# Performance work log

Measured on AMD Instinct MI355X. Metric: run time of the kernel, lower is better.

The kernel has to match this reference:

```python
import jax, jax.numpy as jnp
import numpy as np

N = 20000          # num_node
E = 160000         # num edges (avg degree 8)
IN_N = 64          # in_features_node
IN_E = 32          # in_features_edge
HN = 64            # nhid_node
HE = 64            # nhid_edge
KAPPA = 0.9
ITERS = 8          # fixed Picard iterations for the equilibrium solve


def setup_inputs() -> dict:
    key = jax.random.key(0)
    ks = jax.random.split(key, 16)
    f32 = jnp.float32

    def w(k, shape, fan_in):
        return (jax.random.normal(k, shape, dtype=f32) / np.sqrt(fan_in)).astype(f32)

    return {
        # graph structure (int constants)
        "R": jax.random.randint(ks[0], (E,), 0, N),   # receiver node per edge
        "S": jax.random.randint(ks[1], (E,), 0, N),   # sender node per edge
        "H": jax.random.randint(ks[2], (E,), 0, N),   # edge->node aggregation index
        # features (features-first layout, as in the torch code)
        "node_data": jax.random.normal(ks[3], (IN_N, N), dtype=f32),
        "Ra_data": jax.random.normal(ks[4], (IN_E, E), dtype=f32),
        # INECN_Layer parameters
        "W_es": w(ks[5], (HE, HN), HN),      # sender-message weight
        "W_er": w(ks[6], (HE, HN), HN),      # receiver-message weight
        "Omega_e": w(ks[7], (HE, IN_E), IN_E),
        "Wn": w(ks[8], (HN, HN), HN),        # implicit node-state weight
        "Bm": w(ks[9], (HN, HE), HE),        # edge->node mixing
        "Omega_n": w(ks[10], (HN, IN_N), IN_N),
        # dense head (V_0: nhid->nhid, V_1: nhid->in_features_node)
        "V0_w": w(ks[11], (HN, HN), HN),
        "V0_b": jnp.zeros((HN,), dtype=f32),
        "V1_w": w(ks[12], (IN_N, HN), HN),
        "V1_b": jnp.zeros((IN_N,), dtype=f32),
    }


def reference(R, S, H, node_data, Ra_data, W_es, W_er, Omega_e, Wn, Bm,
              Omega_n, V0_w, V0_b, V1_w, V1_b):
    # spectral-norm style contraction: ||kappa * Wn / ||Wn|||| <= kappa (adj_rho = 1)
    Wn_hat = (KAPPA * Wn) / jnp.maximum(jnp.linalg.norm(Wn), 1.0)

    bias_e = Omega_e @ Ra_data        # [HE, E] injected edge features
    bias_n = Omega_n @ node_data      # [HN, N] injected node features

    def step(X, _):
        # edge update: messages from sender/receiver node states
        He_logits = W_es @ X[:, S] + W_er @ X[:, R] + bias_e      # [HE, E]
        He = jax.nn.relu(He_logits)
        # aggregate edge states back to nodes
        agg = jax.ops.segment_sum(He.T, H, num_segments=N).T      # [HE, N] -> [HE, N]
        # implicit node update (contraction => convergent fixed point)
        X_new = jax.nn.relu(Wn_hat @ X + Bm @ agg + bias_n)       # [HN, N]
        return X_new, None

    X0 = jnp.zeros((HN, N), dtype=node_data.dtype)
    X, _ = jax.lax.scan(step, X0, None, length=ITERS)

    # final edge states / logits at the (approximate) fixed point
    He_logits3 = W_es @ X[:, S] + W_er @ X[:, R] + bias_e         # [HE, E]
    He = jax.nn.relu(He_logits3)

    # dense head: x = V_1(dropout(relu(V_0(x.T))))  (eval mode: dropout = identity)
    x = X.T                                                        # [N, HN]
    x = jax.nn.relu(x @ V0_w.T + V0_b)                             # [N, HN]
    x = x @ V1_w.T + V1_b                                          # [N, IN_N]
    return (x, He, He_logits3)
```

## Files before the change

kernel.cpp:

```cpp
#include <hip/hip_runtime.h>
#include <math.h>

#define KAPPA 0.9f
#define ST 68
#define TN 32

typedef unsigned short u16;

__device__ __forceinline__ float relu_f(float v) { return fmaxf(v, 0.0f); }
__device__ __forceinline__ float bf_lo(unsigned u) { return __uint_as_float(u << 16); }
__device__ __forceinline__ float bf_hi(unsigned u) { return __uint_as_float(u & 0xFFFF0000u); }
__device__ __forceinline__ u16 f2bf(float x) {
  unsigned u = __float_as_uint(x);
  return (u16)((u + 0x7FFFu + ((u >> 16) & 1u)) >> 16);
}
__device__ __forceinline__ unsigned pack2(float a, float b) {
  return (unsigned)f2bf(a) | ((unsigned)f2bf(b) << 16);
}

__global__ __launch_bounds__(256) void wnhat_kernel(const float* __restrict__ Wn,
                                                    float* __restrict__ Wn_hat) {
  __shared__ float red[4];
  int t = threadIdx.x;
  float v[16];
  float s = 0.f;
#pragma unroll
  for (int j = 0; j < 16; ++j) { v[j] = Wn[t + 256 * j]; s += v[j] * v[j]; }
#pragma unroll
  for (int off = 32; off > 0; off >>= 1) s += __shfl_down(s, off, 64);
  if ((t & 63) == 0) red[t >> 6] = s;
  __syncthreads();
  float norm = sqrtf(red[0] + red[1] + red[2] + red[3]);
  float scale = KAPPA / fmaxf(norm, 1.0f);
#pragma unroll
  for (int j = 0; j < 16; ++j) Wn_hat[t + 256 * j] = v[j] * scale;
}

__global__ __launch_bounds__(256) void bias_n_kernel(const float* __restrict__ node_data,
                                                     const float* __restrict__ Om_n,
                                                     float* __restrict__ bias_n, int N) {
  __shared__ float NdT[64][ST];
  __shared__ float Om[64][ST];
  int t = threadIdx.x;
  int n_base = blockIdx.x * 64;
#pragma unroll
  for (int j = 0; j < 16; ++j) {
    int f = t + 256 * j;
    int r = f >> 6, c = f & 63;
    float val = (n_base + c < N) ? node_data[(size_t)r * N + n_base + c] : 0.f;
    NdT[c][r] = val;
    Om[r][c] = Om_n[f];
  }
  __syncthreads();
  int ni = t & 15, h4 = (t >> 4) * 4;
  float acc[4][4] = {};
#pragma unroll 4
  for (int k = 0; k < 64; k += 4) {
    float4 a[4], w[4];
#pragma unroll
    for (int i = 0; i < 4; ++i) a[i] = *(const float4*)&NdT[ni + 16 * i][k];
#pragma unroll
    for (int j = 0; j < 4; ++j) w[j] = *(const float4*)&Om[h4 + j][k];
#pragma unroll
    for (int i = 0; i < 4; ++i)
#pragma unroll
      for (int j = 0; j < 4; ++j)
        acc[i][j] += a[i].x * w[j].x + a[i].y * w[j].y + a[i].z * w[j].z + a[i].w * w[j].w;
  }
#pragma unroll
  for (int i = 0; i < 4; ++i) {
    int n = n_base + ni + 16 * i;
    if (n < N) {
      float4 o = make_float4(acc[i][0], acc[i][1], acc[i][2], acc[i][3]);
      *(float4*)&bias_n[(size_t)n * 64 + h4] = o;
    }
  }
}

__global__ void hist_kernel(const int* __restrict__ H, int* __restrict__ count, int E) {
  int e = blockIdx.x * 256 + threadIdx.x;
  if (e < E) atomicAdd(&count[H[e]], 1);
}

__global__ __launch_bounds__(256) void scan_kernel(int* count, int* row_off, int* cursor,
                                                   int N, int E) {
  __shared__ int offs[256];
  __shared__ int sums[256];
  int t = threadIdx.x;
  int chunk = (N + 255) / 256;
  int lo = t * chunk, hi = min(lo + chunk, N);
  int s = 0;
  for (int n = lo; n < hi; ++n) s += count[n];
  sums[t] = s;
  __syncthreads();
  if (t == 0) {
    int run = 0;
    for (int i = 0; i < 256; ++i) { offs[i] = run; run += sums[i]; }
  }
  __syncthreads();
  int run = offs[t];
  for (int n = lo; n < hi; ++n) {
    int c = count[n];
    row_off[n] = run;
    cursor[n] = run;
    run += c;
  }
  if (t == 0) row_off[N] = E;
}

__global__ void scatter_kernel(const int* __restrict__ H, const int* __restrict__ S,
                               const int* __restrict__ R, int* cursor,
                               int* __restrict__ Ss, int* __restrict__ Rs,
                               int* __restrict__ inv_perm, int E) {
  int e = blockIdx.x * 256 + threadIdx.x;
  if (e < E) {
    int h = H[e];
    int pos = atomicAdd(&cursor[h], 1);
    Ss[pos] = S[e];
    Rs[pos] = R[e];
    inv_perm[e] = pos;
  }
}

__global__ __launch_bounds__(256) void bias_build_kernel(const float* __restrict__ Ra,
                                                         const float* __restrict__ Om_e,
                                                         const int* __restrict__ inv_perm,
                                                         u16* __restrict__ bias_sb, int E) {
  __shared__ float OmT[64][36];
  __shared__ float RaT[64][36];
  int t = threadIdx.x;
  int e_base = blockIdx.x * 64;
#pragma unroll
  for (int j = 0; j < 8; ++j) {
    int f = t + 256 * j;
    int r = f >> 5, c = f & 31;
    OmT[r][c] = Om_e[f];
  }
#pragma unroll
  for (int j = 0; j < 8; ++j) {
    int f = t + 256 * j;
    int r = f >> 6, c = f & 63;
    int ee = e_base + c;
    RaT[c][r] = (ee < E) ? Ra[(size_t)r * E + ee] : 0.f;
  }
  __syncthreads();
  int ei = t & 15, h4 = (t >> 4) * 4;
  float acc[4][4] = {};
#pragma unroll 4
  for (int jj = 0; jj < 32; jj += 4) {
    float4 ra[4], om[4];
#pragma unroll
    for (int i = 0; i < 4; ++i) ra[i] = *(const float4*)&RaT[ei + 16 * i][jj];
#pragma unroll
    for (int j = 0; j < 4; ++j) om[j] = *(const float4*)&OmT[h4 + j][jj];
#pragma unroll
    for (int i = 0; i < 4; ++i)
#pragma unroll
      for (int j = 0; j < 4; ++j)
        acc[i][j] += ra[i].x * om[j].x + ra[i].y * om[j].y + ra[i].z * om[j].z +
                     ra[i].w * om[j].w;
  }
#pragma unroll
  for (int i = 0; i < 4; ++i) {
    int e = e_base + ei + 16 * i;
    if (e < E) {
      int p = inv_perm[e];
      uint2 o;
      o.x = pack2(acc[i][0], acc[i][1]);
      o.y = pack2(acc[i][2], acc[i][3]);
      *(uint2*)&bias_sb[((size_t)p << 6) + h4] = o;
    }
  }
}

template <int FIRST, int LAST>
__global__ __launch_bounds__(256) void iter_kernel(
    const float* __restrict__ X, const u16* __restrict__ MSb_in,
    const u16* __restrict__ MRb_in, const u16* __restrict__ bias_sb,
    const int* __restrict__ Ss, const int* __restrict__ Rs,
    const int* __restrict__ row_off, const float* __restrict__ bias_n,
    const float* __restrict__ Wn_hat, const float* __restrict__ Bm,
    const float* __restrict__ W_es, const float* __restrict__ W_er,
    const float* __restrict__ V0_w, const float* __restrict__ V0_b,
    const float* __restrict__ V1_w, const float* __restrict__ V1_b,
    float* __restrict__ Xout, u16* __restrict__ MSb_out,
    u16* __restrict__ MRb_out, float* __restrict__ head_out, int N) {
  __shared__ float Wa[64][ST], Wb[64][ST];
  __shared__ float Xsh[TN][ST], Ash[TN][ST];
  __shared__ float b0s[64], b1s[64];
  int t = threadIdx.x;
  int n_base = blockIdx.x * TN;
#pragma unroll
  for (int j = 0; j < 16; ++j) {
    int f = t + 256 * j;
    int r = f >> 6, c = f & 63;
    Wa[r][c] = Wn_hat[f];
    Wb[r][c] = Bm[f];
  }
  int n8 = t >> 3;
  int q8 = t & 7;
  int nd = n_base + n8;
  bool ok = nd < N;
  if (!FIRST) {
    float4 x0 = make_float4(0, 0, 0, 0), x1 = x0;
    if (ok) {
      x0 = *(const float4*)&X[(size_t)nd * 64 + q8 * 8];
      x1 = *(const float4*)&X[(size_t)nd * 64 + q8 * 8 + 4];
    }
    *(float4*)&Xsh[n8][q8 * 8] = x0;
    *(float4*)&Xsh[n8][q8 * 8 + 4] = x1;
  }
  float a[8] = {};
  if (ok) {
    int r0 = row_off[nd], r1 = row_off[nd + 1];
    for (int p = r0; p < r1; ++p) {
      uint4 bv = *(const uint4*)&bias_sb[((size_t)p << 6) + q8 * 8];
      if (FIRST) {
        a[0] += relu_f(bf_lo(bv.x)); a[1] += relu_f(bf_hi(bv.x));
        a[2] += relu_f(bf_lo(bv.y)); a[3] += relu_f(bf_hi(bv.y));
        a[4] += relu_f(bf_lo(bv.z)); a[5] += relu_f(bf_hi(bv.z));
        a[6] += relu_f(bf_lo(bv.w)); a[7] += relu_f(bf_hi(bv.w));
      } else {
        int s = Ss[p], r = Rs[p];
        uint4 mv = *(const uint4*)&MSb_in[((size_t)s << 6) + q8 * 8];
        uint4 rv = *(const uint4*)&MRb_in[((size_t)r << 6) + q8 * 8];
        a[0] += relu_f(bf_lo(mv.x) + bf_lo(rv.x) + bf_lo(bv.x));
        a[1] += relu_f(bf_hi(mv.x) + bf_hi(rv.x) + bf_hi(bv.x));
        a[2] += relu_f(bf_lo(mv.y) + bf_lo(rv.y) + bf_lo(bv.y));
        a[3] += relu_f(bf_hi(mv.y) + bf_hi(rv.y) + bf_hi(bv.y));
        a[4] += relu_f(bf_lo(mv.z) + bf_lo(rv.z) + bf_lo(bv.z));
        a[5] += relu_f(bf_hi(mv.z) + bf_hi(rv.z) + bf_hi(bv.z));
        a[6] += relu_f(bf_lo(mv.w) + bf_lo(rv.w) + bf_lo(bv.w));
        a[7] += relu_f(bf_hi(mv.w) + bf_hi(rv.w) + bf_hi(bv.w));
      }
    }
  }
  *(float4*)&Ash[n8][q8 * 8] = make_float4(a[0], a[1], a[2], a[3]);
  *(float4*)&Ash[n8][q8 * 8 + 4] = make_float4(a[4], a[5], a[6], a[7]);
  __syncthreads();
  int ni = t & 15, h4 = (t >> 4) * 4;
  float acc[2][4] = {};
#pragma unroll 4
  for (int k = 0; k < 64; k += 4) {
    float4 xv[2], av[2], wv[4], bv[4];
#pragma unroll
    for (int i = 0; i < 2; ++i) {
      if (!FIRST) xv[i] = *(const float4*)&Xsh[ni + 16 * i][k];
      av[i] = *(const float4*)&Ash[ni + 16 * i][k];
    }
#pragma unroll
    for (int j = 0; j < 4; ++j) {
      wv[j] = *(const float4*)&Wa[h4 + j][k];
      bv[j] = *(const float4*)&Wb[h4 + j][k];
    }
#pragma unroll
    for (int i = 0; i < 2; ++i)
#pragma unroll
      for (int j = 0; j < 4; ++j) {
        float v = av[i].x * bv[j].x + av[i].y * bv[j].y + av[i].z * bv[j].z +
                  av[i].w * bv[j].w;
        if (!FIRST)
          v += xv[i].x * wv[j].x + xv[i].y * wv[j].y + xv[i].z * wv[j].z +
               xv[i].w * wv[j].w;
        acc[i][j] += v;
      }
  }
  __syncthreads();
#pragma unroll
  for (int i = 0; i < 2; ++i) {
    int nn = n_base + ni + 16 * i;
    float4 bb = make_float4(0, 0, 0, 0);
    if (nn < N) bb = *(const float4*)&bias_n[(size_t)nn * 64 + h4];
    float x0 = relu_f(acc[i][0] + bb.x);
    float x1 = relu_f(acc[i][1] + bb.y);
    float x2 = relu_f(acc[i][2] + bb.z);
    float x3 = relu_f(acc[i][3] + bb.w);
    if (!LAST && nn < N)
      *(float4*)&Xout[(size_t)nn * 64 + h4] = make_float4(x0, x1, x2, x3);
    *(float4*)&Xsh[ni + 16 * i][h4] = make_float4(x0, x1, x2, x3);
  }
#pragma unroll
  for (int j = 0; j < 16; ++j) {
    int f = t + 256 * j;
    int r = f >> 6, c = f & 63;
    Wa[r][c] = W_es[f];
    Wb[r][c] = W_er[f];
  }
  __syncthreads();
  {
    float ma[2][4] = {}, ra[2][4] = {};
#pragma unroll 4
    for (int k = 0; k < 64; k += 4) {
      float4 xv[2], ws[4], wr[4];
#pragma unroll
      for (int i = 0; i < 2; ++i) xv[i] = *(const float4*)&Xsh[ni + 16 * i][k];
#pragma unroll
      for (int j = 0; j < 4; ++j) {
        ws[j] = *(const float4*)&Wa[h4 + j][k];
        wr[j] = *(const float4*)&Wb[h4 + j][k];
      }
#pragma unroll
      for (int i = 0; i < 2; ++i)
#pragma unroll
        for (int j = 0; j < 4; ++j) {
          ma[i][j] += xv[i].x * ws[j].x + xv[i].y * ws[j].y + xv[i].z * ws[j].z +
                      xv[i].w * ws[j].w;
          ra[i][j] += xv[i].x * wr[j].x + xv[i].y * wr[j].y + xv[i].z * wr[j].z +
                      xv[i].w * wr[j].w;
        }
    }
#pragma unroll
    for (int i = 0; i < 2; ++i) {
      int nn = n_base + ni + 16 * i;
      if (nn < N) {
        uint2 om, orr;
        om.x = pack2(ma[i][0], ma[i][1]);
        om.y = pack2(ma[i][2], ma[i][3]);
        orr.x = pack2(ra[i][0], ra[i][1]);
        orr.y = pack2(ra[i][2], ra[i][3]);
        *(uint2*)&MSb_out[((size_t)nn << 6) + h4] = om;
        *(uint2*)&MRb_out[((size_t)nn << 6) + h4] = orr;
      }
    }
  }
  if (LAST) {
    __syncthreads();
#pragma unroll
    for (int j = 0; j < 16; ++j) {
      int f = t + 256 * j;
      int r = f >> 6, c = f & 63;
      Wa[r][c] = V0_w[f];
      Wb[r][c] = V1_w[f];
    }
    if (t < 64) b0s[t] = V0_b[t];
    else if (t < 128) b1s[t - 64] = V1_b[t - 64];
    __syncthreads();
    float c1[2][4] = {};
#pragma unroll 4
    for (int k = 0; k < 64; k += 4) {
      float4 xv[2], wv[4];
#pragma unroll
      for (int i = 0; i < 2; ++i) xv[i] = *(const float4*)&Xsh[ni + 16 * i][k];
#pragma unroll
      for (int j = 0; j < 4; ++j) wv[j] = *(const float4*)&Wa[h4 + j][k];
#pragma unroll
      for (int i = 0; i < 2; ++i)
#pragma unroll
        for (int j = 0; j < 4; ++j)
          c1[i][j] += xv[i].x * wv[j].x + xv[i].y * wv[j].y + xv[i].z * wv[j].z +
                      xv[i].w * wv[j].w;
    }
    __syncthreads();
#pragma unroll
    for (int i = 0; i < 2; ++i) {
      float4 o;
      o.x = relu_f(c1[i][0] + b0s[h4 + 0]);
      o.y = relu_f(c1[i][1] + b0s[h4 + 1]);
      o.z = relu_f(c1[i][2] + b0s[h4 + 2]);
      o.w = relu_f(c1[i][3] + b0s[h4 + 3]);
      *(float4*)&Xsh[ni + 16 * i][h4] = o;
    }
    __syncthreads();
    float c2[2][4] = {};
#pragma unroll 4
    for (int k = 0; k < 64; k += 4) {
      float4 xv[2], wv[4];
#pragma unroll
      for (int i = 0; i < 2; ++i) xv[i] = *(const float4*)&Xsh[ni + 16 * i][k];
#pragma unroll
      for (int j = 0; j < 4; ++j) wv[j] = *(const float4*)&Wb[h4 + j][k];
#pragma unroll
      for (int i = 0; i < 2; ++i)
#pragma unroll
        for (int j = 0; j < 4; ++j)
          c2[i][j] += xv[i].x * wv[j].x + xv[i].y * wv[j].y + xv[i].z * wv[j].z +
                      xv[i].w * wv[j].w;
    }
#pragma unroll
    for (int i = 0; i < 2; ++i) {
      int nn = n_base + ni + 16 * i;
      if (nn < N) {
        float4 o;
        o.x = c2[i][0] + b1s[h4 + 0];
        o.y = c2[i][1] + b1s[h4 + 1];
        o.z = c2[i][2] + b1s[h4 + 2];
        o.w = c2[i][3] + b1s[h4 + 3];
        *(float4*)&head_out[(size_t)nn * 64 + h4] = o;
      }
    }
  }
}

__global__ __launch_bounds__(256) void edge_final_kernel(
    const u16* __restrict__ MSb, const u16* __restrict__ MRb,
    const int* __restrict__ S, const int* __restrict__ R,
    const float* __restrict__ Om_e, const float* __restrict__ Ra,
    float* __restrict__ He_out, float* __restrict__ Hel_out, int E) {
  __shared__ float T[64][ST];
  __shared__ float pool2[4608];
  int t = threadIdx.x;
  int e_base = blockIdx.x * 64;
#pragma unroll
  for (int j = 0; j < 8; ++j) {
    int f = t + 256 * j;
    int r = f >> 5, c = f & 31;
    pool2[r * 36 + c] = Om_e[f];
  }
#pragma unroll
  for (int j = 0; j < 8; ++j) {
    int f = t + 256 * j;
    int r = f >> 6, c = f & 63;
    int e2 = e_base + c;
    pool2[2304 + c * 36 + r] = (e2 < E) ? Ra[(size_t)r * E + e2] : 0.f;
  }
  {
    int e = t >> 2, q = t & 3;
    int ee = e_base + e;
    int ec = (ee < E) ? ee : 0;
    int s = S[ec], r = R[ec];
    const u16* mp = &MSb[((size_t)s << 6) + q * 16];
    const u16* rp = &MRb[((size_t)r << 6) + q * 16];
    uint4 m0 = *(const uint4*)mp;
    uint4 m1 = *(const uint4*)(mp + 8);
    uint4 r0 = *(const uint4*)rp;
    uint4 r1 = *(const uint4*)(rp + 8);
    float* tp = &T[e][q * 16];
    tp[0] = bf_lo(m0.x) + bf_lo(r0.x);
    tp[1] = bf_hi(m0.x) + bf_hi(r0.x);
    tp[2] = bf_lo(m0.y) + bf_lo(r0.y);
    tp[3] = bf_hi(m0.y) + bf_hi(r0.y);
    tp[4] = bf_lo(m0.z) + bf_lo(r0.z);
    tp[5] = bf_hi(m0.z) + bf_hi(r0.z);
    tp[6] = bf_lo(m0.w) + bf_lo(r0.w);
    tp[7] = bf_hi(m0.w) + bf_hi(r0.w);
    tp[8] = bf_lo(m1.x) + bf_lo(r1.x);
    tp[9] = bf_hi(m1.x) + bf_hi(r1.x);
    tp[10] = bf_lo(m1.y) + bf_lo(r1.y);
    tp[11] = bf_hi(m1.y) + bf_hi(r1.y);
    tp[12] = bf_lo(m1.z) + bf_lo(r1.z);
    tp[13] = bf_hi(m1.z) + bf_hi(r1.z);
    tp[14] = bf_lo(m1.w) + bf_lo(r1.w);
    tp[15] = bf_hi(m1.w) + bf_hi(r1.w);
  }
  __syncthreads();
  int ei = t & 15, h4 = (t >> 4) * 4;
  float acc[4][4] = {};
#pragma unroll 4
  for (int jj = 0; jj < 32; jj += 4) {
    float4 ra[4], om[4];
#pragma unroll
    for (int i = 0; i < 4; ++i)
      ra[i] = *(const float4*)&pool2[2304 + (ei + 16 * i) * 36 + jj];
#pragma unroll
    for (int j = 0; j < 4; ++j) om[j] = *(const float4*)&pool2[(h4 + j) * 36 + jj];
#pragma unroll
    for (int i = 0; i < 4; ++i)
#pragma unroll
      for (int j = 0; j < 4; ++j)
        acc[i][j] += ra[i].x * om[j].x + ra[i].y * om[j].y + ra[i].z * om[j].z +
                     ra[i].w * om[j].w;
  }
#pragma unroll
  for (int i = 0; i < 4; ++i) {
    float4 tv = *(const float4*)&T[ei + 16 * i][h4];
    acc[i][0] += tv.x;
    acc[i][1] += tv.y;
    acc[i][2] += tv.z;
    acc[i][3] += tv.w;
  }
  __syncthreads();
#pragma unroll
  for (int i = 0; i < 4; ++i)
#pragma unroll
    for (int j = 0; j < 4; ++j)
      pool2[(ei + 16 * i) * 65 + h4 + j] = acc[i][j];
  __syncthreads();
  {
    int e4 = (t & 15) * 4, h0 = t >> 4;
#pragma unroll
    for (int rep = 0; rep < 4; ++rep) {
      int h = h0 + 16 * rep;
      float4 v;
      v.x = pool2[(e4 + 0) * 65 + h];
      v.y = pool2[(e4 + 1) * 65 + h];
      v.z = pool2[(e4 + 2) * 65 + h];
      v.w = pool2[(e4 + 3) * 65 + h];
      size_t idx = (size_t)h * E + e_base + e4;
      if (e_base + e4 < E) {
        *(float4*)&Hel_out[idx] = v;
        float4 u = make_float4(relu_f(v.x), relu_f(v.y), relu_f(v.z), relu_f(v.w));
        *(float4*)&He_out[idx] = u;
      }
    }
  }
}

extern "C" void kernel_launch(void* const* d_in, const int* in_sizes, int n_in,
                              void* d_out, int out_size, void* d_ws, size_t ws_size,
                              hipStream_t stream) {
  const int* R = (const int*)d_in[0];
  const int* S = (const int*)d_in[1];
  const int* H = (const int*)d_in[2];
  const float* node_data = (const float*)d_in[3];
  const float* Ra = (const float*)d_in[4];
  const float* W_es = (const float*)d_in[5];
  const float* W_er = (const float*)d_in[6];
  const float* Om_e = (const float*)d_in[7];
  const float* Wn = (const float*)d_in[8];
  const float* Bm = (const float*)d_in[9];
  const float* Om_n = (const float*)d_in[10];
  const float* V0_w = (const float*)d_in[11];
  const float* V0_b = (const float*)d_in[12];
  const float* V1_w = (const float*)d_in[13];
  const float* V1_b = (const float*)d_in[14];
  const int E = in_sizes[0];
  const int N = in_sizes[3] / 64;
  const size_t N64 = (size_t)N * 64;

  float* ws = (float*)d_ws;
  float* Wn_hat = ws;
  float* bias_n = Wn_hat + 4096;
  float* X0 = bias_n + N64;
  float* X1p = X0 + N64;
  u16* MSb_B = (u16*)(X1p + N64);
  u16* MRb_B = MSb_B + N64;
  int* row_off = (int*)(MRb_B + N64);
  int* cursor = row_off + (N + 1);
  int* Ss = cursor + N;
  int* Rs = Ss + E;
  int* inv_perm = Rs + E;

  float* out = (float*)d_out;
  float* out_x = out;
  float* out_He = out + N64;
  float* out_Hel = out_He + (size_t)64 * E;
  u16* bias_sb = (u16*)out_He;
  u16* MSb_A = (u16*)out_Hel;
  u16* MRb_A = MSb_A + N64;

  int nb_node = (N + 63) / 64;
  int nb_iter = (N + TN - 1) / TN;
  int nb_edge = (E + 63) / 64;
  int nb_flat = (E + 255) / 256;

  hipMemsetAsync(cursor, 0, (size_t)N * sizeof(int), stream);
  wnhat_kernel<<<1, 256, 0, stream>>>(Wn, Wn_hat);
  bias_n_kernel<<<nb_node, 256, 0, stream>>>(node_data, Om_n, bias_n, N);
  hist_kernel<<<nb_flat, 256, 0, stream>>>(H, cursor, E);
  scan_kernel<<<1, 256, 0, stream>>>(cursor, row_off, cursor, N, E);
  scatter_kernel<<<nb_flat, 256, 0, stream>>>(H, S, R, cursor, Ss, Rs, inv_perm, E);
  bias_build_kernel<<<nb_edge, 256, 0, stream>>>(Ra, Om_e, inv_perm, bias_sb, E);

  float* Xa = X0;
  float* Xb = X1p;
  const u16* msi = nullptr;
  const u16* mri = nullptr;
  for (int it = 0; it < 8; ++it) {
    u16* mso = (it & 1) ? MSb_B : MSb_A;
    u16* mro = (it & 1) ? MRb_B : MRb_A;
    if (it == 0)
      iter_kernel<1, 0><<<nb_iter, 256, 0, stream>>>(
          Xa, nullptr, nullptr, bias_sb, Ss, Rs, row_off, bias_n, Wn_hat, Bm, W_es, W_er,
          V0_w, V0_b, V1_w, V1_b, Xb, mso, mro, out_x, N);
    else if (it < 7)
      iter_kernel<0, 0><<<nb_iter, 256, 0, stream>>>(
          Xa, msi, mri, bias_sb, Ss, Rs, row_off, bias_n, Wn_hat, Bm, W_es, W_er,
          V0_w, V0_b, V1_w, V1_b, Xb, mso, mro, out_x, N);
    else
      iter_kernel<0, 1><<<nb_iter, 256, 0, stream>>>(
          Xa, msi, mri, bias_sb, Ss, Rs, row_off, bias_n, Wn_hat, Bm, W_es, W_er,
          V0_w, V0_b, V1_w, V1_b, Xb, mso, mro, out_x, N);
    msi = mso;
    mri = mro;
    float* tmp = Xa; Xa = Xb; Xb = tmp;
  }
  edge_final_kernel<<<nb_edge, 256, 0, stream>>>(MSb_B, MRb_B, S, R, Om_e, Ra,
                                                 out_He, out_Hel, E);
}
```

Measured before the change: 486.3 us.

## Split edge aggregation into separate kernel with 4-way per-node edge parallelism

Moves the per-node gather/relu/sum over incoming edges out of the fused iteration kernel into a dedicated aggregation kernel. That kernel gives each node 32 threads, splits its edge list four ways and reduces the partial sums in shared memory, so more gather loads are in flight. It writes an fp32 agg buffer that the node kernel then reads. Sender and receiver indices are also packed into one int2 array. The cost is an extra launch and an extra global round-trip of the agg buffer per iteration.

```diff
diff --git a/kernel.cpp b/kernel.cpp
--- a/kernel.cpp
+++ b/kernel.cpp
@@ -110,14 +110,12 @@
 
 __global__ void scatter_kernel(const int* __restrict__ H, const int* __restrict__ S,
                                const int* __restrict__ R, int* cursor,
-                               int* __restrict__ Ss, int* __restrict__ Rs,
-                               int* __restrict__ inv_perm, int E) {
+                               int2* __restrict__ SRs, int* __restrict__ inv_perm, int E) {
   int e = blockIdx.x * 256 + threadIdx.x;
   if (e < E) {
     int h = H[e];
     int pos = atomicAdd(&cursor[h], 1);
-    Ss[pos] = S[e];
-    Rs[pos] = R[e];
+    SRs[pos] = make_int2(S[e], R[e]);
     inv_perm[e] = pos;
   }
 }
@@ -173,18 +171,67 @@
   }
 }
 
+template <int FIRST>
+__global__ __launch_bounds__(256) void agg_kernel(
+    const u16* __restrict__ MSb_in, const u16* __restrict__ MRb_in,
+    const u16* __restrict__ bias_sb, const int2* __restrict__ SRs,
+    const int* __restrict__ row_off, float* __restrict__ agg, int N) {
+  __shared__ float part[4][8][ST];
+  int t = threadIdx.x;
+  int nl = t >> 5, sp = (t >> 3) & 3, q8 = t & 7;
+  int nd = blockIdx.x * 8 + nl;
+  float a[8] = {};
+  if (nd < N) {
+    int r0 = row_off[nd], r1 = row_off[nd + 1];
+    for (int p = r0 + sp; p < r1; p += 4) {
+      uint4 bv = *(const uint4*)&bias_sb[((size_t)p << 6) + q8 * 8];
+      if (FIRST) {
+        a[0] += relu_f(bf_lo(bv.x)); a[1] += relu_f(bf_hi(bv.x));
+        a[2] += relu_f(bf_lo(bv.y)); a[3] += relu_f(bf_hi(bv.y));
+        a[4] += relu_f(bf_lo(bv.z)); a[5] += relu_f(bf_hi(bv.z));
+        a[6] += relu_f(bf_lo(bv.w)); a[7] += relu_f(bf_hi(bv.w));
+      } else {
+        int2 sr = SRs[p];
+        uint4 mv = *(const uint4*)&MSb_in[((size_t)sr.x << 6) + q8 * 8];
+        uint4 rv = *(const uint4*)&MRb_in[((size_t)sr.y << 6) + q8 * 8];
+        a[0] += relu_f(bf_lo(mv.x) + bf_lo(rv.x) + bf_lo(bv.x));
+        a[1] += relu_f(bf_hi(mv.x) + bf_hi(rv.x) + bf_hi(bv.x));
+        a[2] += relu_f(bf_lo(mv.y) + bf_lo(rv.y) + bf_lo(bv.y));
+        a[3] += relu_f(bf_hi(mv.y) + bf_hi(rv.y) + bf_hi(bv.y));
+        a[4] += relu_f(bf_lo(mv.z) + bf_lo(rv.z) + bf_lo(bv.z));
+        a[5] += relu_f(bf_hi(mv.z) + bf_hi(rv.z) + bf_hi(bv.z));
+        a[6] += relu_f(bf_lo(mv.w) + bf_lo(rv.w) + bf_lo(bv.w));
+        a[7] += relu_f(bf_hi(mv.w) + bf_hi(rv.w) + bf_hi(bv.w));
+      }
+    }
+  }
+  *(float4*)&part[sp][nl][q8 * 8] = make_float4(a[0], a[1], a[2], a[3]);
+  *(float4*)&part[sp][nl][q8 * 8 + 4] = make_float4(a[4], a[5], a[6], a[7]);
+  __syncthreads();
+  if (sp == 0 && nd < N) {
+#pragma unroll
+    for (int u = 0; u < 2; ++u) {
+      float4 s0 = *(const float4*)&part[0][nl][q8 * 8 + 4 * u];
+      float4 s1 = *(const float4*)&part[1][nl][q8 * 8 + 4 * u];
+      float4 s2 = *(const float4*)&part[2][nl][q8 * 8 + 4 * u];
+      float4 s3 = *(const float4*)&part[3][nl][q8 * 8 + 4 * u];
+      float4 o = make_float4(s0.x + s1.x + s2.x + s3.x, s0.y + s1.y + s2.y + s3.y,
+                             s0.z + s1.z + s2.z + s3.z, s0.w + s1.w + s2.w + s3.w);
+      *(float4*)&agg[(size_t)nd * 64 + q8 * 8 + 4 * u] = o;
+    }
+  }
+}
+
 template <int FIRST, int LAST>
-__global__ __launch_bounds__(256) void iter_kernel(
-    const float* __restrict__ X, const u16* __restrict__ MSb_in,
-    const u16* __restrict__ MRb_in, const u16* __restrict__ bias_sb,
-    const int* __restrict__ Ss, const int* __restrict__ Rs,
-    const int* __restrict__ row_off, const float* __restrict__ bias_n,
-    const float* __restrict__ Wn_hat, const float* __restrict__ Bm,
-    const float* __restrict__ W_es, const float* __restrict__ W_er,
-    const float* __restrict__ V0_w, const float* __restrict__ V0_b,
-    const float* __restrict__ V1_w, const float* __restrict__ V1_b,
-    float* __restrict__ Xout, u16* __restrict__ MSb_out,
-    u16* __restrict__ MRb_out, float* __restrict__ head_out, int N) {
+__global__ __launch_bounds__(256) void node_kernel(
+    const float* __restrict__ X, const float* __restrict__ agg,
+    const float* __restrict__ bias_n, const float* __restrict__ Wn_hat,
+    const float* __restrict__ Bm, const float* __restrict__ W_es,
+    const float* __restrict__ W_er, const float* __restrict__ V0_w,
+    const float* __restrict__ V0_b, const float* __restrict__ V1_w,
+    const float* __restrict__ V1_b, float* __restrict__ Xout,
+    u16* __restrict__ MSb_out, u16* __restrict__ MRb_out,
+    float* __restrict__ head_out, int N) {
   __shared__ float Wa[64][ST], Wb[64][ST];
   __shared__ float Xsh[TN][ST], Ash[TN][ST];
   __shared__ float b0s[64], b1s[64];
@@ -210,33 +257,15 @@
     *(float4*)&Xsh[n8][q8 * 8] = x0;
     *(float4*)&Xsh[n8][q8 * 8 + 4] = x1;
   }
-  float a[8] = {};
-  if (ok) {
-    int r0 = row_off[nd], r1 = row_off[nd + 1];
-    for (int p = r0; p < r1; ++p) {
-      uint4 bv = *(const uint4*)&bias_sb[((size_t)p << 6) + q8 * 8];
-      if (FIRST) {
-        a[0] += relu_f(bf_lo(bv.x)); a[1] += relu_f(bf_hi(bv.x));
-        a[2] += relu_f(bf_lo(bv.y)); a[3] += relu_f(bf_hi(bv.y));
-        a[4] += relu_f(bf_lo(bv.z)); a[5] += relu_f(bf_hi(bv.z));
-        a[6] += relu_f(bf_lo(bv.w)); a[7] += relu_f(bf_hi(bv.w));
-      } else {
-        int s = Ss[p], r = Rs[p];
-        uint4 mv = *(const uint4*)&MSb_in[((size_t)s << 6) + q8 * 8];
-        uint4 rv = *(const uint4*)&MRb_in[((size_t)r << 6) + q8 * 8];
-        a[0] += relu_f(bf_lo(mv.x) + bf_lo(rv.x) + bf_lo(bv.x));
-        a[1] += relu_f(bf_hi(mv.x) + bf_hi(rv.x) + bf_hi(bv.x));
-        a[2] += relu_f(bf_lo(mv.y) + bf_lo(rv.y) + bf_lo(bv.y));
-        a[3] += relu_f(bf_hi(mv.y) + bf_hi(rv.y) + bf_hi(bv.y));
-        a[4] += relu_f(bf_lo(mv.z) + bf_lo(rv.z) + bf_lo(bv.z));
-        a[5] += relu_f(bf_hi(mv.z) + bf_hi(rv.z) + bf_hi(bv.z));
-        a[6] += relu_f(bf_lo(mv.w) + bf_lo(rv.w) + bf_lo(bv.w));
-        a[7] += relu_f(bf_hi(mv.w) + bf_hi(rv.w) + bf_hi(bv.w));
-      }
-    }
-  }
-  *(float4*)&Ash[n8][q8 * 8] = make_float4(a[0], a[1], a[2], a[3]);
-  *(float4*)&Ash[n8][q8 * 8 + 4] = make_float4(a[4], a[5], a[6], a[7]);
+  {
+    float4 a0 = make_float4(0, 0, 0, 0), a1 = a0;
+    if (ok) {
+      a0 = *(const float4*)&agg[(size_t)nd * 64 + q8 * 8];
+      a1 = *(const float4*)&agg[(size_t)nd * 64 + q8 * 8 + 4];
+    }
+    *(float4*)&Ash[n8][q8 * 8] = a0;
+    *(float4*)&Ash[n8][q8 * 8 + 4] = a1;
+  }
   __syncthreads();
   int ni = t & 15, h4 = (t >> 4) * 4;
   float acc[2][4] = {};
@@ -526,9 +555,8 @@
   u16* MRb_B = MSb_B + N64;
   int* row_off = (int*)(MRb_B + N64);
   int* cursor = row_off + (N + 1);
-  int* Ss = cursor + N;
-  int* Rs = Ss + E;
-  int* inv_perm = Rs + E;
+  int2* SRs = (int2*)(cursor + N);
+  int* inv_perm = (int*)(SRs + E);
 
   float* out = (float*)d_out;
   float* out_x = out;
@@ -537,9 +565,11 @@
   u16* bias_sb = (u16*)out_He;
   u16* MSb_A = (u16*)out_Hel;
   u16* MRb_A = MSb_A + N64;
+  float* aggf = (float*)(MRb_A + N64);
 
   int nb_node = (N + 63) / 64;
   int nb_iter = (N + TN - 1) / TN;
+  int nb_agg = (N + 7) / 8;
   int nb_edge = (E + 63) / 64;
   int nb_flat = (E + 255) / 256;
 
@@ -548,7 +578,7 @@
   bias_n_kernel<<<nb_node, 256, 0, stream>>>(node_data, Om_n, bias_n, N);
   hist_kernel<<<nb_flat, 256, 0, stream>>>(H, cursor, E);
   scan_kernel<<<1, 256, 0, stream>>>(cursor, row_off, cursor, N, E);
-  scatter_kernel<<<nb_flat, 256, 0, stream>>>(H, S, R, cursor, Ss, Rs, inv_perm, E);
+  scatter_kernel<<<nb_flat, 256, 0, stream>>>(H, S, R, cursor, SRs, inv_perm, E);
   bias_build_kernel<<<nb_edge, 256, 0, stream>>>(Ra, Om_e, inv_perm, bias_sb, E);
 
   float* Xa = X0;
@@ -558,18 +588,25 @@
   for (int it = 0; it < 8; ++it) {
     u16* mso = (it & 1) ? MSb_B : MSb_A;
     u16* mro = (it & 1) ? MRb_B : MRb_A;
-    if (it == 0)
-      iter_kernel<1, 0><<<nb_iter, 256, 0, stream>>>(
-          Xa, nullptr, nullptr, bias_sb, Ss, Rs, row_off, bias_n, Wn_hat, Bm, W_es, W_er,
-          V0_w, V0_b, V1_w, V1_b, Xb, mso, mro, out_x, N);
-    else if (it < 7)
-      iter_kernel<0, 0><<<nb_iter, 256, 0, stream>>>(
-          Xa, msi, mri, bias_sb, Ss, Rs, row_off, bias_n, Wn_hat, Bm, W_es, W_er,
-          V0_w, V0_b, V1_w, V1_b, Xb, mso, mro, out_x, N);
-    else
-      iter_kernel<0, 1><<<nb_iter, 256, 0, stream>>>(
-          Xa, msi, mri, bias_sb, Ss, Rs, row_off, bias_n, Wn_hat, Bm, W_es, W_er,
-          V0_w, V0_b, V1_w, V1_b, Xb, mso, mro, out_x, N);
+    if (it == 0) {
+      agg_kernel<1><<<nb_agg, 256, 0, stream>>>(nullptr, nullptr, bias_sb, SRs,
+                                                row_off, aggf, N);
+      node_kernel<1, 0><<<nb_iter, 256, 0, stream>>>(
+          Xa, aggf, bias_n, Wn_hat, Bm, W_es, W_er, V0_w, V0_b, V1_w, V1_b,
+          Xb, mso, mro, out_x, N);
+    } else if (it < 7) {
+      agg_kernel<0><<<nb_agg, 256, 0, stream>>>(msi, mri, bias_sb, SRs,
+                                                row_off, aggf, N);
+      node_kernel<0, 0><<<nb_iter, 256, 0, stream>>>(
+          Xa, aggf, bias_n, Wn_hat, Bm, W_es, W_er, V0_w, V0_b, V1_w, V1_b,
+          Xb, mso, mro, out_x, N);
+    } else {
+      agg_kernel<0><<<nb_agg, 256, 0, stream>>>(msi, mri, bias_sb, SRs,
+                                                row_off, aggf, N);
+      node_kernel<0, 1><<<nb_iter, 256, 0, stream>>>(
+          Xa, aggf, bias_n, Wn_hat, Bm, W_es, W_er, V0_w, V0_b, V1_w, V1_b,
+          Xb, mso, mro, out_x, N);
+    }
     msi = mso;
     mri = mro;
     float* tmp = Xa; Xa = Xb; Xb = tmp;
```

Measured after the change: 432.4 us. 11.1% less time.
